# Kernel tuning notes

Hardware: AMD Instinct MI355X
Metric: run time of the kernel (lower is better)

## Reference

```python
import jax, jax.numpy as jnp
import numpy as np

B, C, NB, H, W = 4, 128, 4, 256, 256
BT = C // NB  # bottleneck channels = 32
BN1_EPS, BN2_EPS = 1e-5, 1e-3


def setup_inputs() -> dict:
    key = jax.random.key(0)
    ks = jax.random.split(key, 16)
    x = jax.random.normal(ks[0], (B, C, H, W), dtype=jnp.float32)
    w1 = jax.random.normal(ks[1], (BT, C), dtype=jnp.float32) * 0.1
    bn1_gamma = 1.0 + 0.1 * jax.random.normal(ks[2], (BT,), dtype=jnp.float32)
    bn1_beta = 0.1 * jax.random.normal(ks[3], (BT,), dtype=jnp.float32)
    bn1_mean = 0.1 * jax.random.normal(ks[4], (BT,), dtype=jnp.float32)
    bn1_var = 0.5 + jax.random.uniform(ks[5], (BT,), dtype=jnp.float32)
    # learned box extents (vertical x, horizontal y), guaranteed x_max > x_min
    x_min = jax.random.uniform(ks[6], (BT, NB), minval=-100.0, maxval=-2.0)
    x_max = x_min + jax.random.uniform(ks[7], (BT, NB), minval=2.0, maxval=100.0)
    y_min = jax.random.uniform(ks[8], (BT, NB), minval=-100.0, maxval=-2.0)
    y_max = y_min + jax.random.uniform(ks[9], (BT, NB), minval=2.0, maxval=100.0)
    bn2_gamma = 1.0 + 0.1 * jax.random.normal(ks[10], (C,), dtype=jnp.float32)
    bn2_beta = 0.1 * jax.random.normal(ks[11], (C,), dtype=jnp.float32)
    bn2_mean = 0.1 * jax.random.normal(ks[12], (C,), dtype=jnp.float32)
    bn2_var = 0.5 + jax.random.uniform(ks[13], (C,), dtype=jnp.float32)
    return dict(x=x, w1=w1, bn1_gamma=bn1_gamma, bn1_beta=bn1_beta,
                bn1_mean=bn1_mean, bn1_var=bn1_var,
                x_min=x_min, x_max=x_max, y_min=y_min, y_max=y_max,
                bn2_gamma=bn2_gamma, bn2_beta=bn2_beta,
                bn2_mean=bn2_mean, bn2_var=bn2_var)


def _bn(z, gamma, beta, mean, var, eps):
    inv = gamma / jnp.sqrt(var + eps)
    return z * inv[None, :, None, None] + (beta - mean * inv)[None, :, None, None]


def _box_conv(z, x_min, x_max, y_min, y_max):
    """Continuous box-average filter via bilinear sampling of the integral image.
    z: (B, BT, H, W); box params: (BT, NB). Output: (B, BT*NB, H, W)."""
    # zero-padded 2D integral image S[b,c,i,j] = sum z[b,c,:i,:j]  -> (B,BT,H+1,W+1)
    S = jnp.pad(jnp.cumsum(jnp.cumsum(z, axis=2), axis=3),
                ((0, 0), (0, 0), (1, 0), (1, 0)))

    def sample(Sc, u, v):
        # Sc: (B,H+1,W+1); u: (H,), v: (W,) continuous coords into the integral image
        u = jnp.clip(u, 0.0, float(H))
        v = jnp.clip(v, 0.0, float(W))
        i0 = jnp.clip(jnp.floor(u), 0.0, float(H - 1)).astype(jnp.int32)
        j0 = jnp.clip(jnp.floor(v), 0.0, float(W - 1)).astype(jnp.int32)
        wu = u - i0  # fractional weights (carry gradients w.r.t. box params)
        wv = v - j0
        R = Sc[:, i0, :] * (1.0 - wu)[None, :, None] + Sc[:, i0 + 1, :] * wu[None, :, None]
        return R[:, :, j0] * (1.0 - wv)[None, None, :] + R[:, :, j0 + 1] * wv[None, None, :]

    def one_box(Sc, xmn, xmx, ymn, ymx):
        i = jnp.arange(H, dtype=z.dtype)
        j = jnp.arange(W, dtype=z.dtype)
        F11 = sample(Sc, i + xmx, j + ymx)
        F10 = sample(Sc, i + xmx, j + ymn)
        F01 = sample(Sc, i + xmn, j + ymx)
        F00 = sample(Sc, i + xmn, j + ymn)
        area = (xmx - xmn) * (ymx - ymn)
        return (F11 - F10 - F01 + F00) / area  # (B,H,W)

    per_box = jax.vmap(one_box, in_axes=(None, 0, 0, 0, 0))     # over NB
    per_chan = jax.vmap(per_box, in_axes=(1, 0, 0, 0, 0))       # over BT channels
    out = per_chan(S, x_min, x_max, y_min, y_max)               # (BT,NB,B,H,W)
    return out.transpose(2, 0, 1, 3, 4).reshape(z.shape[0], BT * NB, H, W)


def reference(x, w1, bn1_gamma, bn1_beta, bn1_mean, bn1_var,
              x_min, x_max, y_min, y_max,
              bn2_gamma, bn2_beta, bn2_mean, bn2_var):
    # 1x1 conv (no bias)
    h = jnp.einsum('bchw,kc->bkhw', x, w1)
    h = _bn(h, bn1_gamma, bn1_beta, bn1_mean, bn1_var, BN1_EPS)
    h = _box_conv(h, x_min, x_max, y_min, y_max)
    h = _bn(h, bn2_gamma, bn2_beta, bn2_mean, bn2_var, BN2_EPS)
    h = jax.nn.relu(h)
    return jax.nn.relu(x + h)
```

## Files before the change

kernel.cpp:

```cpp
#include <hip/hip_runtime.h>
#include <math.h>

#define BB 4
#define CC 128
#define BT 32
#define NBOX 4
#define HH 256
#define WW 256
#define HW (HH*WW)
#define SP 257
#define SPLANE (SP*SP)
#define NPLANE (BB*BT)
#define CHUNK 32
#define NCHUNK (HH/CHUNK)
#define ROWS 8

__global__ __launch_bounds__(256) void conv_bn1_scan(
        const float* __restrict__ x, const float* __restrict__ w1,
        const float* __restrict__ g1, const float* __restrict__ b1,
        const float* __restrict__ m1, const float* __restrict__ v1,
        float* __restrict__ t) {
    int p4 = blockIdx.x * 1024 + threadIdx.x * 4;
    int b  = p4 >> 16;
    int ij = p4 & 65535;
    const float4* xb = (const float4*)(x + (size_t)b * (CC * HW) + ij);
    float4 acc[BT];
    #pragma unroll
    for (int k = 0; k < BT; ++k) acc[k] = make_float4(0.f, 0.f, 0.f, 0.f);

    #pragma unroll 4
    for (int c = 0; c < CC; ++c) {
        float4 xv = xb[c * (HW / 4)];
        #pragma unroll
        for (int k = 0; k < BT; ++k) {
            float wv = w1[k * CC + c];
            acc[k].x = fmaf(xv.x, wv, acc[k].x);
            acc[k].y = fmaf(xv.y, wv, acc[k].y);
            acc[k].z = fmaf(xv.z, wv, acc[k].z);
            acc[k].w = fmaf(xv.w, wv, acc[k].w);
        }
    }

    #pragma unroll
    for (int k = 0; k < BT; ++k) {
        float inv = g1[k] * __frsqrt_rn(v1[k] + 1e-5f);
        float add = b1[k] - m1[k] * inv;
        acc[k].x = acc[k].x * inv + add;
        acc[k].y = acc[k].y * inv + add;
        acc[k].z = acc[k].z * inv + add;
        acc[k].w = acc[k].w * inv + add;
    }

    int lane = threadIdx.x & 63;
    float4* tb = (float4*)(t + (size_t)b * (BT * HW) + ij);
    #pragma unroll
    for (int k = 0; k < BT; ++k) {
        float4 v = acc[k];
        v.y += v.x; v.z += v.y; v.w += v.z;
        float tot = v.w;
        float sum = tot;
        #pragma unroll
        for (int off = 1; off < 64; off <<= 1) {
            float o = __shfl_up(sum, off, 64);
            if (lane >= off) sum += o;
        }
        float excl = sum - tot;
        v.x += excl; v.y += excl; v.z += excl; v.w += excl;
        tb[k * (HW / 4)] = v;
    }
}

__global__ __launch_bounds__(256) void col_partial(const float* __restrict__ t,
                                                   float* __restrict__ T) {
    int plane = blockIdx.x >> 3;
    int chunk = blockIdx.x & 7;
    int j = threadIdx.x;
    const float* tp = t + (size_t)plane * HW + chunk * CHUNK * WW + j;
    float vals[CHUNK];
    #pragma unroll
    for (int r = 0; r < CHUNK; ++r) vals[r] = tp[r * WW];
    float s = 0.f;
    #pragma unroll
    for (int r = 0; r < CHUNK; ++r) s += vals[r];
    T[blockIdx.x * 256 + j] = s;
}

__global__ __launch_bounds__(256) void col_final(const float* __restrict__ t,
                                                 const float* __restrict__ T,
                                                 float* __restrict__ s) {
    int plane = blockIdx.x >> 3;
    int chunk = blockIdx.x & 7;
    int j = threadIdx.x;
    float off = 0.f;
    for (int c = 0; c < chunk; ++c) off += T[(plane * 8 + c) * 256 + j];
    const float* tp = t + (size_t)plane * HW + chunk * CHUNK * WW + j;
    float* sp = s + (size_t)plane * SPLANE;
    if (chunk == 0) {
        sp[j + 1] = 0.f;
        if (j == 0) sp[0] = 0.f;
    }
    float vals[CHUNK];
    #pragma unroll
    for (int r = 0; r < CHUNK; ++r) vals[r] = tp[r * WW];
    float run = off;
    int rowbase = chunk * CHUNK;
    #pragma unroll
    for (int r = 0; r < CHUNK; ++r) {
        run += vals[r];
        sp[(size_t)(rowbase + r + 1) * SP + j + 1] = run;
        if (j == 0) sp[(size_t)(rowbase + r + 1) * SP] = 0.f;
    }
}

__global__ __launch_bounds__(256) void box_sample(
        const float* __restrict__ s, const float* __restrict__ x,
        const float* __restrict__ xmin, const float* __restrict__ xmax,
        const float* __restrict__ ymin, const float* __restrict__ ymax,
        const float* __restrict__ g2, const float* __restrict__ b2,
        const float* __restrict__ m2, const float* __restrict__ v2,
        float* __restrict__ out) {
    __shared__ float D[ROWS][SP];
    int bid = blockIdx.x;
    int ig = bid & 31;
    int n  = (bid >> 5) & 3;
    int k  = (bid >> 7) & 31;
    int b  = bid >> 12;
    int j  = threadIdx.x;
    int lane = j & 63;
    int wave = j >> 6;
    int kn = k * NBOX + n;
    int ibase = ig * ROWS;
    const float* sp = s + (size_t)(b * BT + k) * SPLANE;

    float xmn = xmin[kn], xmx = xmax[kn], ymn = ymin[kn], ymx = ymax[kn];

    #pragma unroll
    for (int rr = 0; rr < 2; ++rr) {
        int r = wave + rr * 4;
        float fi = (float)(ibase + r);
        float u_hi = fminf(fmaxf(fi + xmx, 0.f), 256.f);
        float u_lo = fminf(fmaxf(fi + xmn, 0.f), 256.f);
        int i1 = (int)fminf(floorf(u_hi), 255.f);
        int i0 = (int)fminf(floorf(u_lo), 255.f);
        float wu1 = u_hi - (float)i1;
        float wu0 = u_lo - (float)i0;
        const float* rA = sp + (size_t)i1 * SP;
        const float* rB = rA + SP;
        const float* rC = sp + (size_t)i0 * SP;
        const float* rD = rC + SP;
        #pragma unroll
        for (int tcol = 0; tcol < 4; ++tcol) {
            int c = lane + tcol * 64;
            D[r][c] = rA[c] * (1.f - wu1) + rB[c] * wu1
                    - rC[c] * (1.f - wu0) - rD[c] * wu0;
        }
        if (lane == 0) {
            int c = 256;
            D[r][c] = rA[c] * (1.f - wu1) + rB[c] * wu1
                    - rC[c] * (1.f - wu0) - rD[c] * wu0;
        }
    }
    __syncthreads();

    float v_hi = fminf(fmaxf((float)j + ymx, 0.f), 256.f);
    float v_lo = fminf(fmaxf((float)j + ymn, 0.f), 256.f);
    int j1 = (int)fminf(floorf(v_hi), 255.f);
    int j0 = (int)fminf(floorf(v_lo), 255.f);
    float wv1 = v_hi - (float)j1;
    float wv0 = v_lo - (float)j0;
    float cv1 = 1.f - wv1;
    float cv0 = 1.f - wv0;

    float inv = g2[kn] * __frsqrt_rn(v2[kn] + 1e-3f);
    float scale = inv * __frcp_rn((xmx - xmn) * (ymx - ymn));
    float add = b2[kn] - m2[kn] * inv;

    int obase = ((b * CC + kn) * HH + ibase) * WW + j;
    const float* xp = x + obase;
    float* op = out + obase;
    #pragma unroll
    for (int r = 0; r < ROWS; ++r) {
        float hi = D[r][j1] * cv1 + D[r][j1 + 1] * wv1;
        float lo = D[r][j0] * cv0 + D[r][j0 + 1] * wv0;
        float val = (hi - lo) * scale + add;
        val = fmaxf(val, 0.f);
        float xv = __builtin_nontemporal_load(xp + r * WW);
        __builtin_nontemporal_store(fmaxf(xv + val, 0.f), op + r * WW);
    }
}

extern "C" void kernel_launch(void* const* d_in, const int* in_sizes, int n_in,
                              void* d_out, int out_size, void* d_ws, size_t ws_size,
                              hipStream_t stream) {
    const float* x    = (const float*)d_in[0];
    const float* w1   = (const float*)d_in[1];
    const float* g1   = (const float*)d_in[2];
    const float* b1   = (const float*)d_in[3];
    const float* m1   = (const float*)d_in[4];
    const float* v1   = (const float*)d_in[5];
    const float* xmin = (const float*)d_in[6];
    const float* xmax = (const float*)d_in[7];
    const float* ymin = (const float*)d_in[8];
    const float* ymax = (const float*)d_in[9];
    const float* g2   = (const float*)d_in[10];
    const float* b2   = (const float*)d_in[11];
    const float* m2   = (const float*)d_in[12];
    const float* v2   = (const float*)d_in[13];
    float* out = (float*)d_out;

    float* h = (float*)d_ws;
    float* S = h + (size_t)BB * BT * HW;
    float* T = S + (size_t)NPLANE * SPLANE;

    conv_bn1_scan<<<(BB * HW) / 1024, 256, 0, stream>>>(x, w1, g1, b1, m1, v1, h);
    col_partial  <<<NPLANE * NCHUNK, 256, 0, stream>>>(h, T);
    col_final    <<<NPLANE * NCHUNK, 256, 0, stream>>>(h, T, S);
    box_sample   <<<BB * BT * NBOX * (HH / ROWS), 256, 0, stream>>>(
                     S, x, xmin, xmax, ymin, ymax, g2, b2, m2, v2, out);
}
```

Before: 327.8 us.

## Vectorize column scan, enlarge box_sample row tile, prefetch residual input

The column scan kernels now process four columns per thread with float4 loads and run one 64-thread wave per block instead of 256 threads. box_sample handles 16 rows per block instead of 8, which halves the block count, and issues the residual x loads before building the shared row differences so that latency overlaps. The conv loop unroll goes from 4 to 8. Costs include higher register pressure from 16 prefetched values and larger shared memory per block, and the scan launches give less parallelism per block.

```diff
diff --git a/kernel.cpp b/kernel.cpp
--- a/kernel.cpp
+++ b/kernel.cpp
@@ -13,7 +13,7 @@
 #define NPLANE (BB*BT)
 #define CHUNK 32
 #define NCHUNK (HH/CHUNK)
-#define ROWS 8
+#define ROWS 16
 
 __global__ __launch_bounds__(256) void conv_bn1_scan(
         const float* __restrict__ x, const float* __restrict__ w1,
@@ -28,7 +28,7 @@
     #pragma unroll
     for (int k = 0; k < BT; ++k) acc[k] = make_float4(0.f, 0.f, 0.f, 0.f);
 
-    #pragma unroll 4
+    #pragma unroll 8
     for (int c = 0; c < CC; ++c) {
         float4 xv = xb[c * (HW / 4)];
         #pragma unroll
@@ -70,45 +70,55 @@
     }
 }
 
-__global__ __launch_bounds__(256) void col_partial(const float* __restrict__ t,
-                                                   float* __restrict__ T) {
+__global__ __launch_bounds__(64) void col_partial(const float* __restrict__ t,
+                                                  float* __restrict__ T) {
     int plane = blockIdx.x >> 3;
     int chunk = blockIdx.x & 7;
-    int j = threadIdx.x;
-    const float* tp = t + (size_t)plane * HW + chunk * CHUNK * WW + j;
-    float vals[CHUNK];
-    #pragma unroll
-    for (int r = 0; r < CHUNK; ++r) vals[r] = tp[r * WW];
-    float s = 0.f;
-    #pragma unroll
-    for (int r = 0; r < CHUNK; ++r) s += vals[r];
-    T[blockIdx.x * 256 + j] = s;
-}
-
-__global__ __launch_bounds__(256) void col_final(const float* __restrict__ t,
-                                                 const float* __restrict__ T,
-                                                 float* __restrict__ s) {
+    int q = threadIdx.x;
+    const float4* tp = (const float4*)(t + (size_t)plane * HW + chunk * CHUNK * WW) + q;
+    float4 vals[CHUNK];
+    #pragma unroll
+    for (int r = 0; r < CHUNK; ++r) vals[r] = tp[r * (WW / 4)];
+    float4 s = make_float4(0.f, 0.f, 0.f, 0.f);
+    #pragma unroll
+    for (int r = 0; r < CHUNK; ++r) {
+        s.x += vals[r].x; s.y += vals[r].y; s.z += vals[r].z; s.w += vals[r].w;
+    }
+    ((float4*)(T + blockIdx.x * 256))[q] = s;
+}
+
+__global__ __launch_bounds__(64) void col_final(const float* __restrict__ t,
+                                                const float* __restrict__ T,
+                                                float* __restrict__ s) {
     int plane = blockIdx.x >> 3;
     int chunk = blockIdx.x & 7;
-    int j = threadIdx.x;
-    float off = 0.f;
-    for (int c = 0; c < chunk; ++c) off += T[(plane * 8 + c) * 256 + j];
-    const float* tp = t + (size_t)plane * HW + chunk * CHUNK * WW + j;
+    int q = threadIdx.x;
+    float4 off = make_float4(0.f, 0.f, 0.f, 0.f);
+    for (int c = 0; c < chunk; ++c) {
+        float4 tv = ((const float4*)(T + (plane * 8 + c) * 256))[q];
+        off.x += tv.x; off.y += tv.y; off.z += tv.z; off.w += tv.w;
+    }
+    const float4* tp = (const float4*)(t + (size_t)plane * HW + chunk * CHUNK * WW) + q;
     float* sp = s + (size_t)plane * SPLANE;
     if (chunk == 0) {
-        sp[j + 1] = 0.f;
-        if (j == 0) sp[0] = 0.f;
-    }
-    float vals[CHUNK];
-    #pragma unroll
-    for (int r = 0; r < CHUNK; ++r) vals[r] = tp[r * WW];
-    float run = off;
+        #pragma unroll
+        for (int e = 0; e < 4; ++e) sp[4 * q + 1 + e] = 0.f;
+        if (q == 0) sp[0] = 0.f;
+    }
+    float4 vals[CHUNK];
+    #pragma unroll
+    for (int r = 0; r < CHUNK; ++r) vals[r] = tp[r * (WW / 4)];
+    float4 run = off;
     int rowbase = chunk * CHUNK;
     #pragma unroll
     for (int r = 0; r < CHUNK; ++r) {
-        run += vals[r];
-        sp[(size_t)(rowbase + r + 1) * SP + j + 1] = run;
-        if (j == 0) sp[(size_t)(rowbase + r + 1) * SP] = 0.f;
+        run.x += vals[r].x; run.y += vals[r].y; run.z += vals[r].z; run.w += vals[r].w;
+        float* row = sp + (size_t)(rowbase + r + 1) * SP;
+        row[4 * q + 1] = run.x;
+        row[4 * q + 2] = run.y;
+        row[4 * q + 3] = run.z;
+        row[4 * q + 4] = run.w;
+        if (q == 0) row[0] = 0.f;
     }
 }
 
@@ -121,10 +131,10 @@
         float* __restrict__ out) {
     __shared__ float D[ROWS][SP];
     int bid = blockIdx.x;
-    int ig = bid & 31;
-    int n  = (bid >> 5) & 3;
-    int k  = (bid >> 7) & 31;
-    int b  = bid >> 12;
+    int ig = bid & 15;
+    int n  = (bid >> 4) & 3;
+    int k  = (bid >> 6) & 31;
+    int b  = bid >> 11;
     int j  = threadIdx.x;
     int lane = j & 63;
     int wave = j >> 6;
@@ -134,8 +144,14 @@
 
     float xmn = xmin[kn], xmx = xmax[kn], ymn = ymin[kn], ymx = ymax[kn];
 
-    #pragma unroll
-    for (int rr = 0; rr < 2; ++rr) {
+    int obase = ((b * CC + kn) * HH + ibase) * WW + j;
+    const float* xp = x + obase;
+    float xv[ROWS];
+    #pragma unroll
+    for (int r = 0; r < ROWS; ++r) xv[r] = __builtin_nontemporal_load(xp + r * WW);
+
+    #pragma unroll
+    for (int rr = 0; rr < 4; ++rr) {
         int r = wave + rr * 4;
         float fi = (float)(ibase + r);
         float u_hi = fminf(fmaxf(fi + xmx, 0.f), 256.f);
@@ -175,8 +191,6 @@
     float scale = inv * __frcp_rn((xmx - xmn) * (ymx - ymn));
     float add = b2[kn] - m2[kn] * inv;
 
-    int obase = ((b * CC + kn) * HH + ibase) * WW + j;
-    const float* xp = x + obase;
     float* op = out + obase;
     #pragma unroll
     for (int r = 0; r < ROWS; ++r) {
@@ -184,8 +198,7 @@
         float lo = D[r][j0] * cv0 + D[r][j0 + 1] * wv0;
         float val = (hi - lo) * scale + add;
         val = fmaxf(val, 0.f);
-        float xv = __builtin_nontemporal_load(xp + r * WW);
-        __builtin_nontemporal_store(fmaxf(xv + val, 0.f), op + r * WW);
+        __builtin_nontemporal_store(fmaxf(xv[r] + val, 0.f), op + r * WW);
     }
 }
 
@@ -213,8 +226,8 @@
     float* T = S + (size_t)NPLANE * SPLANE;
 
     conv_bn1_scan<<<(BB * HW) / 1024, 256, 0, stream>>>(x, w1, g1, b1, m1, v1, h);
-    col_partial  <<<NPLANE * NCHUNK, 256, 0, stream>>>(h, T);
-    col_final    <<<NPLANE * NCHUNK, 256, 0, stream>>>(h, T, S);
+    col_partial  <<<NPLANE * NCHUNK, 64, 0, stream>>>(h, T);
+    col_final    <<<NPLANE * NCHUNK, 64, 0, stream>>>(h, T, S);
     box_sample   <<<BB * BT * NBOX * (HH / ROWS), 256, 0, stream>>>(
                      S, x, xmin, xmax, ymin, ymax, g2, b2, m2, v2, out);
 }
```

Measured after the change: 348.0 us. 6.2% more time.
